# Kernel optimization log

Hardware: AMD Instinct MI355X
Metric: run time of the kernel (lower is better)

## Reference

```python
import jax, jax.numpy as jnp
import numpy as np
import math

DIM = 512
B, L = 32, 2048
NEG = jnp.float32(-2**32 + 1)  # padding value used by the torch module

def setup_inputs() -> dict:
    key = jax.random.key(0)
    k1, k2, k3, k4 = jax.random.split(key, 4)
    Ez = jax.random.normal(k1, (B, L, DIM), dtype=jnp.float32)
    # 6 Linear(dim, dim, bias=False) layers each for Q, K, V; weight is [out, in]
    s = 1.0 / math.sqrt(DIM)
    Wq = jax.random.uniform(k2, (6, DIM, DIM), dtype=jnp.float32, minval=-s, maxval=s)
    Wk = jax.random.uniform(k3, (6, DIM, DIM), dtype=jnp.float32, minval=-s, maxval=s)
    Wv = jax.random.uniform(k4, (6, DIM, DIM), dtype=jnp.float32, minval=-s, maxval=s)
    return {"Ez": Ez, "Wq": Wq, "Wk": Wk, "Wv": Wv, "z": 3}

def reference(Ez, Wq, Wk, Wv, z):
    dim = Ez.shape[-1]
    # nn.Linear: x @ W.T
    q = jnp.einsum('bld,ed->ble', Ez, Wq[z])
    k = jnp.einsum('bld,ed->ble', Ez, Wk[z])
    v = jnp.einsum('bld,ed->ble', Ez, Wv[z])
    scores = jnp.einsum('bqe,bke->bqk', q, k) / jnp.float32(math.sqrt(dim))
    Lq = scores.shape[-1]
    tril = jnp.tril(jnp.ones((Lq, Lq), dtype=jnp.float32))  # causal mask
    scores = jnp.where(tril[None, :, :] == 0, NEG, scores)
    attn = jax.nn.softmax(scores, axis=-1)
    return jnp.einsum('bqk,bke->bqe', attn, v)
```

## Files before the change

### kernel.cpp

```cpp
#include <hip/hip_runtime.h>
#include <hip/hip_bf16.h>


typedef __attribute__((ext_vector_type(8))) short short8;
typedef __attribute__((ext_vector_type(4))) short short4v;
typedef __attribute__((ext_vector_type(4))) float f32x4;

#define DIM 512
#define LSEQ 2048
#define NB 32
#define SCALE 0.04419417382415922f
#define LOG2E 1.4426950408889634f

__device__ __forceinline__ short f2bs(float f) {
  __hip_bfloat16 h = __float2bfloat16(f);
  return __builtin_bit_cast(short, h);
}

__device__ __forceinline__ void gld16(const void* g, void* l) {
  __builtin_amdgcn_global_load_lds(
      (const unsigned int __attribute__((address_space(1)))*)g,
      (unsigned int __attribute__((address_space(3)))*)l, 16, 0, 0);
}

__global__ __launch_bounds__(256) void wcvt_kernel(
    const float* __restrict__ Wq, const float* __restrict__ Wk,
    const float* __restrict__ Wv, const int* __restrict__ zp,
    short* __restrict__ Wb) {
  int z = *zp;
  int i = blockIdx.x * 256 + threadIdx.x;
  int g = i >> 15;
  int off = (i & 32767) * 8;
  int n = off >> 9, d0 = off & 511;
  int kt = d0 >> 5, c = d0 & 31;
  int sw = ((c >> 3) ^ ((n >> 1) & 3));
  const float* src = (g == 0 ? Wq : (g == 1 ? Wk : Wv)) + (size_t)z * DIM * DIM + off;
  float4 a = *(const float4*)src, b = *(const float4*)(src + 4);
  short8 v;
  v[0]=f2bs(a.x); v[1]=f2bs(a.y); v[2]=f2bs(a.z); v[3]=f2bs(a.w);
  v[4]=f2bs(b.x); v[5]=f2bs(b.y); v[6]=f2bs(b.z); v[7]=f2bs(b.w);
  *(short8*)&Wb[((size_t)(g * 16 + kt) * 512 + n) * 32 + sw * 8] = v;
}

__global__ __launch_bounds__(512, 4) void proj_kernel(
    const float* __restrict__ Ez, const short* __restrict__ Wb,
    short* __restrict__ Qb, short* __restrict__ Kb, short* __restrict__ Vtb) {
  int g = blockIdx.z;
  const short* W = Wb + (size_t)g * 16 * 512 * 32;
  __shared__ short As[2][64 * 32];
  __shared__ short Bs[2][512 * 32];
  int tid = threadIdx.x, lane = tid & 63, wid = tid >> 6;
  int l15 = lane & 15, lg = lane >> 4;
  int m0 = blockIdx.x * 64;
  int sw = (l15 >> 1) & 3;
  f32x4 zero4 = {0.f, 0.f, 0.f, 0.f};
  f32x4 acc[4][4];
  #pragma unroll
  for (int mi = 0; mi < 4; mi++)
    #pragma unroll
    for (int ni = 0; ni < 4; ni++) acc[mi][ni] = zero4;

  int arow = tid >> 3, aq = tid & 7;
  int aoff = arow * 32 + (((aq >> 1) ^ ((arow >> 1) & 3)) << 3) + (aq & 1) * 4;
  const float* aptr = Ez + (size_t)(m0 + arow) * DIM + aq * 4;

  {
    float4 a = *(const float4*)aptr;
    short4v av;
    av[0]=f2bs(a.x); av[1]=f2bs(a.y); av[2]=f2bs(a.z); av[3]=f2bs(a.w);
    *(short4v*)&As[0][aoff] = av;
    #pragma unroll
    for (int ii = 0; ii < 4; ii++) {
      int s = wid * 4 + ii;
      gld16(W + s * 512 + lane * 8, &Bs[0][s * 512]);
    }
  }
  __syncthreads();

  #pragma unroll 2
  for (int kt = 0; kt < 16; kt++) {
    int cur = kt & 1;
    float4 a;
    if (kt < 15) {
      a = *(const float4*)(aptr + (kt + 1) * 32);
      #pragma unroll
      for (int ii = 0; ii < 4; ii++) {
        int s = wid * 4 + ii;
        gld16(W + (size_t)(kt + 1) * 16384 + s * 512 + lane * 8, &Bs[cur ^ 1][s * 512]);
      }
    }
    short8 af[4], bf[4];
    #pragma unroll
    for (int mi = 0; mi < 4; mi++)
      af[mi] = *(const short8*)&As[cur][(mi * 16 + l15) * 32 + ((lg ^ sw) << 3)];
    #pragma unroll
    for (int ni = 0; ni < 4; ni++)
      bf[ni] = *(const short8*)&Bs[cur][(wid * 64 + ni * 16 + l15) * 32 + ((lg ^ sw) << 3)];
    __builtin_amdgcn_s_setprio(1);
    #pragma unroll
    for (int mi = 0; mi < 4; mi++)
      #pragma unroll
      for (int ni = 0; ni < 4; ni++)
        acc[mi][ni] = __builtin_amdgcn_mfma_f32_16x16x32_bf16(af[mi], bf[ni], acc[mi][ni], 0, 0, 0);
    __builtin_amdgcn_s_setprio(0);
    if (kt < 15) {
      short4v av;
      av[0]=f2bs(a.x); av[1]=f2bs(a.y); av[2]=f2bs(a.z); av[3]=f2bs(a.w);
      *(short4v*)&As[cur ^ 1][aoff] = av;
    }
    __syncthreads();
  }

  if (g == 2) {
    #pragma unroll
    for (int mi = 0; mi < 4; mi++) {
      int gm0 = m0 + mi * 16 + lg * 4;
      int b = gm0 >> 11, l0 = gm0 & (LSEQ - 1);
      int t = l0 >> 5, c0 = l0 & 31;
      #pragma unroll
      for (int ni = 0; ni < 4; ni++) {
        int e = wid * 64 + ni * 16 + l15;
        short4v v;
        v[0]=f2bs(acc[mi][ni][0]); v[1]=f2bs(acc[mi][ni][1]);
        v[2]=f2bs(acc[mi][ni][2]); v[3]=f2bs(acc[mi][ni][3]);
        size_t idx = ((size_t)(b * 64 + t) * 512 + e) * 32
                     + (((c0 >> 3) ^ ((e >> 1) & 3)) << 3) + (c0 & 7);
        *(short4v*)&Vtb[idx] = v;
      }
    }
  } else {
    short* dst = (g == 0 ? Qb : Kb);
    float sc = (g == 0 ? SCALE * LOG2E : 1.0f);
    #pragma unroll
    for (int mi = 0; mi < 4; mi++) {
      int gm0 = m0 + mi * 16 + lg * 4;
      #pragma unroll
      for (int ni = 0; ni < 4; ni++) {
        int gn = wid * 64 + ni * 16 + l15;
        #pragma unroll
        for (int r = 0; r < 4; r++)
          dst[(size_t)(gm0 + r) * DIM + gn] = f2bs(acc[mi][ni][r] * sc);
      }
    }
  }
}

__device__ __forceinline__ void stage_k(const short* __restrict__ Kb,
                                        short* Klbuf,
                                        int batch, int t, int wid, int lane) {
  #pragma unroll
  for (int ii = 0; ii < 4; ii++) {
    int r = wid + ii * 8;
    const short* src = Kb + (size_t)(batch * LSEQ + t * 32 + r) * DIM + ((lane ^ wid) * 8);
    gld16(src, Klbuf + r * 512);
  }
}
__device__ __forceinline__ void stage_v(const short* __restrict__ Vtb,
                                        short* Vlbuf,
                                        int batch, int t, int wid, int lane) {
  const short* vt = Vtb + (size_t)(batch * 64 + t) * 16384;
  #pragma unroll
  for (int ii = 0; ii < 4; ii++) {
    int s = wid * 4 + ii;
    gld16(vt + s * 512 + lane * 8, Vlbuf + s * 512);
  }
}

__global__ __launch_bounds__(512, 2) void attn_kernel(
    const short* __restrict__ Qb, const short* __restrict__ Kb,
    const short* __restrict__ Vtb, float* __restrict__ out) {
  __shared__ short Kl[2][32 * 512];
  __shared__ short Vl[2][512 * 32];
  __shared__ short P_lds[8][16][40];
  int tid = threadIdx.x, lane = tid & 63, wid = tid >> 6;
  int l15 = lane & 15, lg = lane >> 4;
  int batch = blockIdx.x;
  f32x4 zero4 = {0.f, 0.f, 0.f, 0.f};
  short8 ones;
  #pragma unroll
  for (int i = 0; i < 8; i++) ones[i] = (short)0x3F80;

  int a0 = (l15 >> 2) & 1, b0 = l15 & 3;
  int kqE = l15 * 512 + 8 * (lg ^ b0) + 32 * a0;
  int kqO = l15 * 512 + 8 * (lg ^ b0) - 32 * a0;
  int voff = l15 * 32 + 8 * (lg ^ ((l15 >> 1) & 3));
  short* pw = &P_lds[wid][lg * 4][l15];
  const short* pr = &P_lds[wid][l15][lg * 8];

  for (int qpass = 0; qpass < 2; qpass++) {
    int qt = qpass ? (int)blockIdx.y : 15 - (int)blockIdx.y;
    int qb0 = qt * 128;
    int q0w = qb0 + wid * 16;
    int nt = qt * 4 + 4;

    stage_k(Kb, Kl[0], batch, 0, wid, lane);

    const short* qrow = Qb + (size_t)(batch * LSEQ + q0w + l15) * DIM;
    short8 qf[16];
    #pragma unroll
    for (int kt = 0; kt < 16; kt++) qf[kt] = *(const short8*)(qrow + kt * 32 + lg * 8);

    f32x4 oacc[32];
    #pragma unroll
    for (int i = 0; i < 32; i++) oacc[i] = zero4;
    f32x4 dacc = zero4;
    float mrun = -1e30f;
    short8 pa;

    __syncthreads();

    for (int t = 0; t < nt; t++) {
      int cur = t & 1;
      if (t + 1 < nt)
        stage_k(Kb, Kl[cur ^ 1], batch, t + 1, wid, lane);
      stage_v(Vtb, Vl[cur], batch, t, wid, lane);

      bool act = (t * 32 <= q0w + 15);
      bool actp = (t > 0) && ((t - 1) * 32 <= q0w + 15);
      f32x4 sacc[2] = {zero4, zero4};
      if (act && actp) {
        const short* pE = Kl[cur] + kqE;
        const short* pO = Kl[cur] + kqO;
        const short* vb = Vl[cur ^ 1] + voff;
        __builtin_amdgcn_s_setprio(1);
        dacc = __builtin_amdgcn_mfma_f32_16x16x32_bf16(pa, ones, dacc, 0, 0, 0);
        #pragma unroll
        for (int kt = 0; kt < 16; kt += 2) {
          short8 k0 = *(const short8*)(pE + 32 * kt);
          short8 k1 = *(const short8*)(pE + 8192 + 32 * kt);
          sacc[0] = __builtin_amdgcn_mfma_f32_16x16x32_bf16(qf[kt], k0, sacc[0], 0, 0, 0);
          sacc[1] = __builtin_amdgcn_mfma_f32_16x16x32_bf16(qf[kt], k1, sacc[1], 0, 0, 0);
          short8 v0 = *(const short8*)(vb + (kt * 2) * 512);
          short8 v1 = *(const short8*)(vb + (kt * 2 + 1) * 512);
          oacc[kt * 2] = __builtin_amdgcn_mfma_f32_16x16x32_bf16(pa, v0, oacc[kt * 2], 0, 0, 0);
          oacc[kt * 2 + 1] = __builtin_amdgcn_mfma_f32_16x16x32_bf16(pa, v1, oacc[kt * 2 + 1], 0, 0, 0);
          short8 k2 = *(const short8*)(pO + 32 * (kt + 1));
          short8 k3 = *(const short8*)(pO + 8192 + 32 * (kt + 1));
          sacc[0] = __builtin_amdgcn_mfma_f32_16x16x32_bf16(qf[kt + 1], k2, sacc[0], 0, 0, 0);
          sacc[1] = __builtin_amdgcn_mfma_f32_16x16x32_bf16(qf[kt + 1], k3, sacc[1], 0, 0, 0);
          short8 v2 = *(const short8*)(vb + (kt * 2 + 2) * 512);
          short8 v3 = *(const short8*)(vb + (kt * 2 + 3) * 512);
          oacc[kt * 2 + 2] = __builtin_amdgcn_mfma_f32_16x16x32_bf16(pa, v2, oacc[kt * 2 + 2], 0, 0, 0);
          oacc[kt * 2 + 3] = __builtin_amdgcn_mfma_f32_16x16x32_bf16(pa, v3, oacc[kt * 2 + 3], 0, 0, 0);
        }
        __builtin_amdgcn_s_setprio(0);
      } else if (act) {
        const short* pE = Kl[cur] + kqE;
        const short* pO = Kl[cur] + kqO;
        __builtin_amdgcn_s_setprio(1);
        #pragma unroll
        for (int kt = 0; kt < 16; kt += 2) {
          short8 k0 = *(const short8*)(pE + 32 * kt);
          short8 k1 = *(const short8*)(pE + 8192 + 32 * kt);
          sacc[0] = __builtin_amdgcn_mfma_f32_16x16x32_bf16(qf[kt], k0, sacc[0], 0, 0, 0);
          sacc[1] = __builtin_amdgcn_mfma_f32_16x16x32_bf16(qf[kt], k1, sacc[1], 0, 0, 0);
          short8 k2 = *(const short8*)(pO + 32 * (kt + 1));
          short8 k3 = *(const short8*)(pO + 8192 + 32 * (kt + 1));
          sacc[0] = __builtin_amdgcn_mfma_f32_16x16x32_bf16(qf[kt + 1], k2, sacc[0], 0, 0, 0);
          sacc[1] = __builtin_amdgcn_mfma_f32_16x16x32_bf16(qf[kt + 1], k3, sacc[1], 0, 0, 0);
        }
        __builtin_amdgcn_s_setprio(0);
      } else if (actp) {
        const short* vb = Vl[cur ^ 1] + voff;
        __builtin_amdgcn_s_setprio(1);
        dacc = __builtin_amdgcn_mfma_f32_16x16x32_bf16(pa, ones, dacc, 0, 0, 0);
        #pragma unroll
        for (int et = 0; et < 32; et++) {
          short8 bv = *(const short8*)(vb + et * 512);
          oacc[et] = __builtin_amdgcn_mfma_f32_16x16x32_bf16(pa, bv, oacc[et], 0, 0, 0);
        }
        __builtin_amdgcn_s_setprio(0);
      }
      if (act) {
        if (t * 32 + 31 > q0w) {
          #pragma unroll
          for (int r = 0; r < 4; r++) {
            int q = q0w + lg * 4 + r;
            if (t * 32 + l15 > q) sacc[0][r] = -1e30f;
            if (t * 32 + 16 + l15 > q) sacc[1][r] = -1e30f;
          }
        }
        float lm = fmaxf(
            fmaxf(fmaxf(sacc[0][0], sacc[0][1]), fmaxf(sacc[0][2], sacc[0][3])),
            fmaxf(fmaxf(sacc[1][0], sacc[1][1]), fmaxf(sacc[1][2], sacc[1][3])));
        if (__any(lm > mrun + 11.5f)) {
          float mx = lm;
          #pragma unroll
          for (int off = 1; off < 64; off <<= 1) mx = fmaxf(mx, __shfl_xor(mx, off, 64));
          float alpha = exp2f(mrun - mx);
          mrun = mx;
          dacc[0] *= alpha; dacc[1] *= alpha; dacc[2] *= alpha; dacc[3] *= alpha;
          #pragma unroll
          for (int et = 0; et < 32; et++) {
            oacc[et][0] *= alpha; oacc[et][1] *= alpha;
            oacc[et][2] *= alpha; oacc[et][3] *= alpha;
          }
        }
        #pragma unroll
        for (int r = 0; r < 4; r++) {
          pw[r * 40] = f2bs(exp2f(sacc[0][r] - mrun));
          pw[r * 40 + 16] = f2bs(exp2f(sacc[1][r] - mrun));
        }
        pa = *(const short8*)pr;
      }
      __syncthreads();
    }
    if ((nt - 1) * 32 <= q0w + 15) {
      const short* vb = Vl[(nt - 1) & 1] + voff;
      dacc = __builtin_amdgcn_mfma_f32_16x16x32_bf16(pa, ones, dacc, 0, 0, 0);
      #pragma unroll
      for (int et = 0; et < 32; et++) {
        short8 bv = *(const short8*)(vb + et * 512);
        oacc[et] = __builtin_amdgcn_mfma_f32_16x16x32_bf16(pa, bv, oacc[et], 0, 0, 0);
      }
    }
    float inv[4];
    #pragma unroll
    for (int r = 0; r < 4; r++) inv[r] = 1.0f / dacc[r];
    #pragma unroll
    for (int et = 0; et < 32; et++)
      #pragma unroll
      for (int r = 0; r < 4; r++) {
        int q = q0w + lg * 4 + r;
        out[((size_t)(batch * LSEQ + q)) * DIM + et * 16 + l15] = oacc[et][r] * inv[r];
      }
    __syncthreads();
  }
}

extern "C" void kernel_launch(void* const* d_in, const int* in_sizes, int n_in,
                              void* d_out, int out_size, void* d_ws, size_t ws_size,
                              hipStream_t stream) {
  const float* Ez = (const float*)d_in[0];
  const float* Wq = (const float*)d_in[1];
  const float* Wk = (const float*)d_in[2];
  const float* Wv = (const float*)d_in[3];
  const int* zp = (const int*)d_in[4];
  float* out = (float*)d_out;
  short* Qb = (short*)d_ws;
  short* Kb = Qb + (size_t)NB * LSEQ * DIM;
  short* Vtb = Kb + (size_t)NB * LSEQ * DIM;
  short* Wb = (short*)d_out;
  hipLaunchKernelGGL(wcvt_kernel, dim3(384), dim3(256), 0, stream,
                     Wq, Wk, Wv, zp, Wb);
  hipLaunchKernelGGL(proj_kernel, dim3(1024, 1, 3), dim3(512), 0, stream,
                     Ez, Wb, Qb, Kb, Vtb);
  hipLaunchKernelGGL(attn_kernel, dim3(32, 8), dim3(512), 0, stream,
                     Qb, Kb, Vtb, out);
}
```

Baseline: 420.0 us.

## Split PV output columns across waves with shared P tiles in LDS

The PV stage is repartitioned so each wave owns a 64-column slice of the output for all 128 query rows, instead of all 512 columns for its own 16 rows. P tiles and per-wave rescale factors are double-buffered in LDS so every wave can read all eight row-blocks' probabilities, and row sums are combined through LDS at the end. This spreads the PV work evenly across waves, so the causal skip no longer leaves some waves idle, and cuts the V LDS reads each wave issues. In exchange it adds more LDS traffic for P and alpha, per-tile rescale branches, and a larger LDS footprint.

```diff
diff --git a/kernel.cpp b/kernel.cpp
--- a/kernel.cpp
+++ b/kernel.cpp
@@ -171,7 +171,9 @@
     const short* __restrict__ Vtb, float* __restrict__ out) {
   __shared__ short Kl[2][32 * 512];
   __shared__ short Vl[2][512 * 32];
-  __shared__ short P_lds[8][16][40];
+  __shared__ short P_lds[2][8][16][40];
+  __shared__ float alpha_lds[2][8];
+  __shared__ float dsum[128];
   int tid = threadIdx.x, lane = tid & 63, wid = tid >> 6;
   int l15 = lane & 15, lg = lane >> 4;
   int batch = blockIdx.x;
@@ -183,9 +185,9 @@
   int a0 = (l15 >> 2) & 1, b0 = l15 & 3;
   int kqE = l15 * 512 + 8 * (lg ^ b0) + 32 * a0;
   int kqO = l15 * 512 + 8 * (lg ^ b0) - 32 * a0;
-  int voff = l15 * 32 + 8 * (lg ^ ((l15 >> 1) & 3));
-  short* pw = &P_lds[wid][lg * 4][l15];
-  const short* pr = &P_lds[wid][l15][lg * 8];
+  int voff = wid * 2048 + l15 * 32 + 8 * (lg ^ ((l15 >> 1) & 3));
+  short* pw = &P_lds[0][wid][lg * 4][l15];
+  const short* prd = &P_lds[0][0][l15][lg * 8];
 
   for (int qpass = 0; qpass < 2; qpass++) {
     int qt = qpass ? (int)blockIdx.y : 15 - (int)blockIdx.y;
@@ -200,48 +202,91 @@
     #pragma unroll
     for (int kt = 0; kt < 16; kt++) qf[kt] = *(const short8*)(qrow + kt * 32 + lg * 8);
 
-    f32x4 oacc[32];
-    #pragma unroll
-    for (int i = 0; i < 32; i++) oacc[i] = zero4;
+    f32x4 oacc[8][4];
+    #pragma unroll
+    for (int i = 0; i < 8; i++)
+      #pragma unroll
+      for (int j = 0; j < 4; j++) oacc[i][j] = zero4;
     f32x4 dacc = zero4;
     float mrun = -1e30f;
-    short8 pa;
 
     __syncthreads();
 
     for (int t = 0; t < nt; t++) {
-      int cur = t & 1;
+      int cur = t & 1, pb = cur ^ 1;
       if (t + 1 < nt)
         stage_k(Kb, Kl[cur ^ 1], batch, t + 1, wid, lane);
       stage_v(Vtb, Vl[cur], batch, t, wid, lane);
 
       bool act = (t * 32 <= q0w + 15);
-      bool actp = (t > 0) && ((t - 1) * 32 <= q0w + 15);
       f32x4 sacc[2] = {zero4, zero4};
-      if (act && actp) {
-        const short* pE = Kl[cur] + kqE;
-        const short* pO = Kl[cur] + kqO;
-        const short* vb = Vl[cur ^ 1] + voff;
+
+      if (t > 0) {
+        bool pvact[8];
+        float af8[8];
+        #pragma unroll
+        for (int j = 0; j < 8; j++) {
+          pvact[j] = ((t - 1) * 32 <= qb0 + j * 16 + 15);
+          af8[j] = alpha_lds[pb][j];
+        }
+        const short* vb = Vl[pb] + voff;
+        const short* pbase = prd + pb * 5120;
         __builtin_amdgcn_s_setprio(1);
-        dacc = __builtin_amdgcn_mfma_f32_16x16x32_bf16(pa, ones, dacc, 0, 0, 0);
-        #pragma unroll
-        for (int kt = 0; kt < 16; kt += 2) {
-          short8 k0 = *(const short8*)(pE + 32 * kt);
-          short8 k1 = *(const short8*)(pE + 8192 + 32 * kt);
-          sacc[0] = __builtin_amdgcn_mfma_f32_16x16x32_bf16(qf[kt], k0, sacc[0], 0, 0, 0);
-          sacc[1] = __builtin_amdgcn_mfma_f32_16x16x32_bf16(qf[kt], k1, sacc[1], 0, 0, 0);
-          short8 v0 = *(const short8*)(vb + (kt * 2) * 512);
-          short8 v1 = *(const short8*)(vb + (kt * 2 + 1) * 512);
-          oacc[kt * 2] = __builtin_amdgcn_mfma_f32_16x16x32_bf16(pa, v0, oacc[kt * 2], 0, 0, 0);
-          oacc[kt * 2 + 1] = __builtin_amdgcn_mfma_f32_16x16x32_bf16(pa, v1, oacc[kt * 2 + 1], 0, 0, 0);
-          short8 k2 = *(const short8*)(pO + 32 * (kt + 1));
-          short8 k3 = *(const short8*)(pO + 8192 + 32 * (kt + 1));
-          sacc[0] = __builtin_amdgcn_mfma_f32_16x16x32_bf16(qf[kt + 1], k2, sacc[0], 0, 0, 0);
-          sacc[1] = __builtin_amdgcn_mfma_f32_16x16x32_bf16(qf[kt + 1], k3, sacc[1], 0, 0, 0);
-          short8 v2 = *(const short8*)(vb + (kt * 2 + 2) * 512);
-          short8 v3 = *(const short8*)(vb + (kt * 2 + 3) * 512);
-          oacc[kt * 2 + 2] = __builtin_amdgcn_mfma_f32_16x16x32_bf16(pa, v2, oacc[kt * 2 + 2], 0, 0, 0);
-          oacc[kt * 2 + 3] = __builtin_amdgcn_mfma_f32_16x16x32_bf16(pa, v3, oacc[kt * 2 + 3], 0, 0, 0);
+        if (pvact[wid]) {
+          short8 paw = *(const short8*)(pbase + wid * 640);
+          dacc = __builtin_amdgcn_mfma_f32_16x16x32_bf16(paw, ones, dacc, 0, 0, 0);
+        }
+        if (act) {
+          const short* pE = Kl[cur] + kqE;
+          const short* pO = Kl[cur] + kqO;
+          #pragma unroll
+          for (int j = 0; j < 8; j++) {
+            int kt = 2 * j;
+            short8 k0 = *(const short8*)(pE + 32 * kt);
+            short8 k1 = *(const short8*)(pE + 8192 + 32 * kt);
+            sacc[0] = __builtin_amdgcn_mfma_f32_16x16x32_bf16(qf[kt], k0, sacc[0], 0, 0, 0);
+            sacc[1] = __builtin_amdgcn_mfma_f32_16x16x32_bf16(qf[kt], k1, sacc[1], 0, 0, 0);
+            if (pvact[j]) {
+              short8 pA = *(const short8*)(pbase + j * 640);
+              float a = af8[j];
+              if (a != 1.0f) {
+                #pragma unroll
+                for (int e4 = 0; e4 < 4; e4++) {
+                  oacc[j][e4][0] *= a; oacc[j][e4][1] *= a;
+                  oacc[j][e4][2] *= a; oacc[j][e4][3] *= a;
+                }
+              }
+              #pragma unroll
+              for (int e4 = 0; e4 < 4; e4++) {
+                short8 bv = *(const short8*)(vb + e4 * 512);
+                oacc[j][e4] = __builtin_amdgcn_mfma_f32_16x16x32_bf16(pA, bv, oacc[j][e4], 0, 0, 0);
+              }
+            }
+            short8 k2 = *(const short8*)(pO + 32 * (kt + 1));
+            short8 k3 = *(const short8*)(pO + 8192 + 32 * (kt + 1));
+            sacc[0] = __builtin_amdgcn_mfma_f32_16x16x32_bf16(qf[kt + 1], k2, sacc[0], 0, 0, 0);
+            sacc[1] = __builtin_amdgcn_mfma_f32_16x16x32_bf16(qf[kt + 1], k3, sacc[1], 0, 0, 0);
+          }
+        } else {
+          #pragma unroll
+          for (int j = 0; j < 8; j++) {
+            if (pvact[j]) {
+              short8 pA = *(const short8*)(pbase + j * 640);
+              float a = af8[j];
+              if (a != 1.0f) {
+                #pragma unroll
+                for (int e4 = 0; e4 < 4; e4++) {
+                  oacc[j][e4][0] *= a; oacc[j][e4][1] *= a;
+                  oacc[j][e4][2] *= a; oacc[j][e4][3] *= a;
+                }
+              }
+              #pragma unroll
+              for (int e4 = 0; e4 < 4; e4++) {
+                short8 bv = *(const short8*)(vb + e4 * 512);
+                oacc[j][e4] = __builtin_amdgcn_mfma_f32_16x16x32_bf16(pA, bv, oacc[j][e4], 0, 0, 0);
+              }
+            }
+          }
         }
         __builtin_amdgcn_s_setprio(0);
       } else if (act) {
@@ -260,17 +305,8 @@
           sacc[1] = __builtin_amdgcn_mfma_f32_16x16x32_bf16(qf[kt + 1], k3, sacc[1], 0, 0, 0);
         }
         __builtin_amdgcn_s_setprio(0);
-      } else if (actp) {
-        const short* vb = Vl[cur ^ 1] + voff;
-        __builtin_amdgcn_s_setprio(1);
-        dacc = __builtin_amdgcn_mfma_f32_16x16x32_bf16(pa, ones, dacc, 0, 0, 0);
-        #pragma unroll
-        for (int et = 0; et < 32; et++) {
-          short8 bv = *(const short8*)(vb + et * 512);
-          oacc[et] = __builtin_amdgcn_mfma_f32_16x16x32_bf16(pa, bv, oacc[et], 0, 0, 0);
-        }
-        __builtin_amdgcn_s_setprio(0);
-      }
+      }
+
       if (act) {
         if (t * 32 + 31 > q0w) {
           #pragma unroll
@@ -283,46 +319,70 @@
         float lm = fmaxf(
             fmaxf(fmaxf(sacc[0][0], sacc[0][1]), fmaxf(sacc[0][2], sacc[0][3])),
             fmaxf(fmaxf(sacc[1][0], sacc[1][1]), fmaxf(sacc[1][2], sacc[1][3])));
+        float alpha_t = 1.0f;
         if (__any(lm > mrun + 11.5f)) {
           float mx = lm;
           #pragma unroll
           for (int off = 1; off < 64; off <<= 1) mx = fmaxf(mx, __shfl_xor(mx, off, 64));
-          float alpha = exp2f(mrun - mx);
+          alpha_t = exp2f(mrun - mx);
           mrun = mx;
-          dacc[0] *= alpha; dacc[1] *= alpha; dacc[2] *= alpha; dacc[3] *= alpha;
-          #pragma unroll
-          for (int et = 0; et < 32; et++) {
-            oacc[et][0] *= alpha; oacc[et][1] *= alpha;
-            oacc[et][2] *= alpha; oacc[et][3] *= alpha;
-          }
-        }
+          dacc[0] *= alpha_t; dacc[1] *= alpha_t;
+          dacc[2] *= alpha_t; dacc[3] *= alpha_t;
+        }
+        int pboff = cur * 5120;
         #pragma unroll
         for (int r = 0; r < 4; r++) {
-          pw[r * 40] = f2bs(exp2f(sacc[0][r] - mrun));
-          pw[r * 40 + 16] = f2bs(exp2f(sacc[1][r] - mrun));
-        }
-        pa = *(const short8*)pr;
+          pw[pboff + r * 40] = f2bs(exp2f(sacc[0][r] - mrun));
+          pw[pboff + r * 40 + 16] = f2bs(exp2f(sacc[1][r] - mrun));
+        }
+        if (lane == 0) alpha_lds[cur][wid] = alpha_t;
       }
       __syncthreads();
     }
-    if ((nt - 1) * 32 <= q0w + 15) {
-      const short* vb = Vl[(nt - 1) & 1] + voff;
-      dacc = __builtin_amdgcn_mfma_f32_16x16x32_bf16(pa, ones, dacc, 0, 0, 0);
-      #pragma unroll
-      for (int et = 0; et < 32; et++) {
-        short8 bv = *(const short8*)(vb + et * 512);
-        oacc[et] = __builtin_amdgcn_mfma_f32_16x16x32_bf16(pa, bv, oacc[et], 0, 0, 0);
-      }
-    }
-    float inv[4];
-    #pragma unroll
-    for (int r = 0; r < 4; r++) inv[r] = 1.0f / dacc[r];
-    #pragma unroll
-    for (int et = 0; et < 32; et++)
+
+    {
+      int pb = (nt - 1) & 1;
+      const short* vb = Vl[pb] + voff;
+      const short* pbase = prd + pb * 5120;
+      if ((nt - 1) * 32 <= q0w + 15) {
+        short8 paw = *(const short8*)(pbase + wid * 640);
+        dacc = __builtin_amdgcn_mfma_f32_16x16x32_bf16(paw, ones, dacc, 0, 0, 0);
+      }
+      #pragma unroll
+      for (int j = 0; j < 8; j++) {
+        if ((nt - 1) * 32 <= qb0 + j * 16 + 15) {
+          short8 pA = *(const short8*)(pbase + j * 640);
+          float a = alpha_lds[pb][j];
+          if (a != 1.0f) {
+            #pragma unroll
+            for (int e4 = 0; e4 < 4; e4++) {
+              oacc[j][e4][0] *= a; oacc[j][e4][1] *= a;
+              oacc[j][e4][2] *= a; oacc[j][e4][3] *= a;
+            }
+          }
+          #pragma unroll
+          for (int e4 = 0; e4 < 4; e4++) {
+            short8 bv = *(const short8*)(vb + e4 * 512);
+            oacc[j][e4] = __builtin_amdgcn_mfma_f32_16x16x32_bf16(pA, bv, oacc[j][e4], 0, 0, 0);
+          }
+        }
+      }
+    }
+    if (l15 == 0) {
+      #pragma unroll
+      for (int r = 0; r < 4; r++) dsum[wid * 16 + lg * 4 + r] = dacc[r];
+    }
+    __syncthreads();
+    #pragma unroll
+    for (int j = 0; j < 8; j++)
       #pragma unroll
       for (int r = 0; r < 4; r++) {
-        int q = q0w + lg * 4 + r;
-        out[((size_t)(batch * LSEQ + q)) * DIM + et * 16 + l15] = oacc[et][r] * inv[r];
+        float inv = 1.0f / dsum[j * 16 + lg * 4 + r];
+        int q = qb0 + j * 16 + lg * 4 + r;
+        #pragma unroll
+        for (int e4 = 0; e4 < 4; e4++)
+          out[((size_t)(batch * LSEQ + q)) * DIM + wid * 64 + e4 * 16 + l15] =
+              oacc[j][e4][r] * inv;
       }
     __syncthreads();
   }
```

Result: slower. 515.5 us (+22.7%).
